# Kernel optimization log

Measured on AMD Instinct MI355X. Metric: run time of the kernel, lower is better.

The kernel has to match this reference:

```python
import jax, jax.numpy as jnp
import numpy as np

B, S, D = 4, 4096, 256

def setup_inputs() -> dict:
    key = jax.random.key(0)
    k1, k2 = jax.random.split(key)
    x = jax.random.normal(k1, (B, S, D), dtype=jnp.float32)
    # xavier_uniform for Linear(D, 2D): bound = sqrt(6/(fan_in+fan_out))
    bound = np.sqrt(6.0 / (D + 2 * D))
    W = jax.random.uniform(k2, (2 * D, D), dtype=jnp.float32, minval=-bound, maxval=bound)
    b = jnp.zeros((2 * D,), dtype=jnp.float32)
    return {"x": x, "W": W, "b": b}

def reference(x, W, b):
    # qk projection: [B,S,2D]
    qk = jnp.einsum('bsd,ed->bse', x, W) + b
    q, k = jnp.split(qk, 2, axis=-1)            # each [B,S,D]
    v = x
    scale = 1.0 / np.sqrt(D)
    logits = jnp.einsum('bqd,bkd->bqk', q, k) * scale   # [B,S,S]
    attn = jax.nn.softmax(logits, axis=-1)
    values = jnp.einsum('bqk,bkd->bqd', attn, v)        # [B,S,D]
    return values.sum(axis=1)                           # [B,D] sum-pool over queries
```

## Files before the change

kernel.cpp:

```cpp
#include <hip/hip_runtime.h>
#include <stdint.h>

typedef __bf16 v8bf __attribute__((ext_vector_type(8)));
typedef float  v4f  __attribute__((ext_vector_type(4)));
typedef int    v4i  __attribute__((ext_vector_type(4)));
typedef unsigned short u16;
typedef unsigned char  u8;

static constexpr int B_ = 4, S_ = 4096, D_ = 256, E_ = 512;
static constexpr float QSC_ = 127.0f / 4.8f;
static constexpr float DQ_  = 1.288045e-4f;

#define AS1C(p) ((const __attribute__((address_space(1))) void*)(p))
#define AS3(p)  ((__attribute__((address_space(3))) void*)(p))

__device__ __forceinline__ v8bf ldfrag(const u16* p) {
    return __builtin_bit_cast(v8bf, *(const uint4*)p);
}
__device__ __forceinline__ u16 f2bf(float f) {
    return __builtin_bit_cast(u16, (__bf16)f);
}
__device__ __forceinline__ u8 f2i8(float f) {
    float t = fminf(fmaxf(f * QSC_, -127.f), 127.f);
    return (u8)(signed char)__float2int_rn(t);
}

__global__ void k_convw(const float* __restrict__ Wf, u16* __restrict__ Wb) {
    int i = blockIdx.x * 256 + threadIdx.x;
    Wb[i] = f2bf(Wf[i]);
}

__global__ __launch_bounds__(256) void k_proj(const float* __restrict__ x,
                                              const u16* __restrict__ Wb,
                                              const float* __restrict__ bias,
                                              u8* __restrict__ Qi,
                                              u8* __restrict__ Ki) {
    const int tid = threadIdx.x, wave = tid >> 6, lane = tid & 63;
    const int l15 = lane & 15, quad = lane >> 4;
    const int tt = blockIdx.x * 2 + (wave >> 1);
    const int wsel = wave & 1;
    const int tbase = tt * 16;

    v8bf a[8];
    const float* xrow = x + (size_t)(tbase + l15) * D_ + quad * 8;
#pragma unroll
    for (int j = 0; j < 8; ++j) {
        float4 f0 = *(const float4*)(xrow + j * 32);
        float4 f1 = *(const float4*)(xrow + j * 32 + 4);
        v8bf t;
        t[0] = (__bf16)f0.x; t[1] = (__bf16)f0.y; t[2] = (__bf16)f0.z; t[3] = (__bf16)f0.w;
        t[4] = (__bf16)f1.x; t[5] = (__bf16)f1.y; t[6] = (__bf16)f1.z; t[7] = (__bf16)f1.w;
        a[j] = t;
    }

    u8* dst = wsel ? Ki : Qi;
    const u16* wbase = Wb + (size_t)(wsel * 256 + l15) * D_ + quad * 8;
    const float* bb = bias + wsel * 256;

    v8bf wcur[8], wnxt[8];
#pragma unroll
    for (int j = 0; j < 8; ++j) wcur[j] = ldfrag(wbase + j * 32);

    auto tile = [&](const v8bf (&wb)[8], int nt) {
        v4f acc = {0.f, 0.f, 0.f, 0.f};
#pragma unroll
        for (int j = 0; j < 8; ++j)
            acc = __builtin_amdgcn_mfma_f32_16x16x32_bf16(a[j], wb[j], acc, 0, 0, 0);
        const int col = nt * 16 + l15;
        const float bv = bb[col];
#pragma unroll
        for (int r = 0; r < 4; ++r) {
            const int tok = tbase + quad * 4 + r;
            dst[tok * D_ + col] = f2i8(acc[r] + bv);
        }
    };

    for (int nt = 0; nt < 16; nt += 2) {
        const u16* wp1 = wbase + (size_t)(nt + 1) * 16 * D_;
#pragma unroll
        for (int j = 0; j < 8; ++j) wnxt[j] = ldfrag(wp1 + j * 32);
        tile(wcur, nt);
        if (nt + 2 < 16) {
            const u16* wp2 = wbase + (size_t)(nt + 2) * 16 * D_;
#pragma unroll
            for (int j = 0; j < 8; ++j) wcur[j] = ldfrag(wp2 + j * 32);
        }
        tile(wnxt, nt + 1);
    }
}

__device__ __forceinline__ void stage64(const u8* src, u8* dst,
                                        int wave, int lane) {
#pragma unroll
    for (int v = 0; v < 4; ++v) {
        const int sbase = v * 256 + wave * 64;
        const int slot = sbase + lane;
        const int R = slot >> 4, P = slot & 15;
        const int c = P ^ (R & 15);
        __builtin_amdgcn_global_load_lds(AS1C(src + R * 256 + c * 16),
                                         AS3(dst + sbase * 16), 16, 0, 0);
    }
}

__global__ __launch_bounds__(256, 2) void k_passA(const u8* __restrict__ Qi,
                                                  const u8* __restrict__ Ki,
                                                  float* __restrict__ Zp) {
    __shared__ u8 sK[2][16384];
    const int tid = threadIdx.x, wave = tid >> 6, lane = tid & 63;
    const int l15 = lane & 15, quad = lane >> 4;
    const int blk = blockIdx.x;
    const int ks = blk & 7;
    const int qg = (blk >> 3) & 15;
    const int b = blk >> 7;
    const int qbase = qg * 256 + wave * 64;
    const int kstart = ks * 512;

    v4i a[4][4];
    {
        const u8* qp = Qi + (size_t)(b * S_ + qbase + l15) * D_ + quad * 16;
#pragma unroll
        for (int s = 0; s < 4; ++s)
#pragma unroll
            for (int c = 0; c < 4; ++c)
                a[s][c] = *(const v4i*)(qp + s * 16 * D_ + c * 64);
    }
    float z[4][4];
#pragma unroll
    for (int s = 0; s < 4; ++s)
#pragma unroll
        for (int r = 0; r < 4; ++r) z[s][r] = 0.f;

    const u8* kb = Ki + (size_t)(b * S_ + kstart) * D_;
    stage64(kb, sK[0], wave, lane);

    for (int t = 0; t < 8; ++t) {
        __syncthreads();
        if (t + 1 < 8) stage64(kb + (size_t)(t + 1) * 64 * D_, sK[(t + 1) & 1], wave, lane);
        const u8* base = sK[t & 1];
#pragma unroll
        for (int u = 0; u < 4; ++u) {
            v4i bf[4];
#pragma unroll
            for (int kc = 0; kc < 4; ++kc) {
                const int P = (kc * 4 + quad) ^ l15;
                bf[kc] = *(const v4i*)(base + (u * 16 + l15) * 256 + P * 16);
            }
            v4i c0 = {0,0,0,0}, c1 = {0,0,0,0}, c2 = {0,0,0,0}, c3 = {0,0,0,0};
#pragma unroll
            for (int kc = 0; kc < 4; ++kc) {
                c0 = __builtin_amdgcn_mfma_i32_16x16x64_i8(a[0][kc], bf[kc], c0, 0, 0, 0);
                c1 = __builtin_amdgcn_mfma_i32_16x16x64_i8(a[1][kc], bf[kc], c1, 0, 0, 0);
                c2 = __builtin_amdgcn_mfma_i32_16x16x64_i8(a[2][kc], bf[kc], c2, 0, 0, 0);
                c3 = __builtin_amdgcn_mfma_i32_16x16x64_i8(a[3][kc], bf[kc], c3, 0, 0, 0);
            }
#pragma unroll
            for (int r = 0; r < 4; ++r) {
                z[0][r] += __builtin_amdgcn_exp2f((float)c0[r] * DQ_);
                z[1][r] += __builtin_amdgcn_exp2f((float)c1[r] * DQ_);
                z[2][r] += __builtin_amdgcn_exp2f((float)c2[r] * DQ_);
                z[3][r] += __builtin_amdgcn_exp2f((float)c3[r] * DQ_);
            }
        }
    }

    float* zdst = Zp + (size_t)ks * B_ * S_ + b * S_ + qbase;
#pragma unroll
    for (int s = 0; s < 4; ++s)
#pragma unroll
        for (int r = 0; r < 4; ++r) {
            float v = z[s][r];
#pragma unroll
            for (int off = 1; off < 16; off <<= 1) v += __shfl_xor(v, off);
            if (l15 == 0) zdst[s * 16 + quad * 4 + r] = v;
        }
}

__global__ __launch_bounds__(256, 2) void k_passB(const u8* __restrict__ Qi,
                                                  const u8* __restrict__ Ki,
                                                  const float* __restrict__ Zp,
                                                  float* __restrict__ wp) {
    __shared__ u8 sQ[2][16384];
    __shared__ float sRZ[512];
    const int tid = threadIdx.x, wave = tid >> 6, lane = tid & 63;
    const int l15 = lane & 15, quad = lane >> 4;
    const int blk = blockIdx.x;
    const int qs = blk & 7;
    const int kg = (blk >> 3) & 15;
    const int b = blk >> 7;
    const int kbase = kg * 256 + wave * 64;
    const int qstart = qs * 512;

    v4i bk[4][4];
    {
        const u8* kp = Ki + (size_t)(b * S_ + kbase + l15) * D_ + quad * 16;
#pragma unroll
        for (int s = 0; s < 4; ++s)
#pragma unroll
            for (int c = 0; c < 4; ++c)
                bk[s][c] = *(const v4i*)(kp + s * 16 * D_ + c * 64);
    }
    float wsum[4] = {0.f, 0.f, 0.f, 0.f};

    const u8* qb = Qi + (size_t)(b * S_ + qstart) * D_;
    stage64(qb, sQ[0], wave, lane);

#pragma unroll
    for (int i = tid; i < 512; i += 256) {
        float zs = 0.f;
#pragma unroll
        for (int p = 0; p < 8; ++p)
            zs += Zp[(size_t)p * B_ * S_ + b * S_ + qstart + i];
        sRZ[i] = __builtin_amdgcn_rcpf(zs);
    }

    for (int t = 0; t < 8; ++t) {
        __syncthreads();
        if (t + 1 < 8) stage64(qb + (size_t)(t + 1) * 64 * D_, sQ[(t + 1) & 1], wave, lane);
        const u8* base = sQ[t & 1];
#pragma unroll
        for (int u = 0; u < 4; ++u) {
            const v4f rzv = *(const v4f*)(&sRZ[t * 64 + u * 16 + quad * 4]);
            v4i af[4];
#pragma unroll
            for (int kc = 0; kc < 4; ++kc) {
                const int P = (kc * 4 + quad) ^ l15;
                af[kc] = *(const v4i*)(base + (u * 16 + l15) * 256 + P * 16);
            }
            v4i c0 = {0,0,0,0}, c1 = {0,0,0,0}, c2 = {0,0,0,0}, c3 = {0,0,0,0};
#pragma unroll
            for (int kc = 0; kc < 4; ++kc) {
                c0 = __builtin_amdgcn_mfma_i32_16x16x64_i8(af[kc], bk[0][kc], c0, 0, 0, 0);
                c1 = __builtin_amdgcn_mfma_i32_16x16x64_i8(af[kc], bk[1][kc], c1, 0, 0, 0);
                c2 = __builtin_amdgcn_mfma_i32_16x16x64_i8(af[kc], bk[2][kc], c2, 0, 0, 0);
                c3 = __builtin_amdgcn_mfma_i32_16x16x64_i8(af[kc], bk[3][kc], c3, 0, 0, 0);
            }
            wsum[0] += __builtin_amdgcn_exp2f((float)c0[0] * DQ_) * rzv[0] + __builtin_amdgcn_exp2f((float)c0[1] * DQ_) * rzv[1]
                     + __builtin_amdgcn_exp2f((float)c0[2] * DQ_) * rzv[2] + __builtin_amdgcn_exp2f((float)c0[3] * DQ_) * rzv[3];
            wsum[1] += __builtin_amdgcn_exp2f((float)c1[0] * DQ_) * rzv[0] + __builtin_amdgcn_exp2f((float)c1[1] * DQ_) * rzv[1]
                     + __builtin_amdgcn_exp2f((float)c1[2] * DQ_) * rzv[2] + __builtin_amdgcn_exp2f((float)c1[3] * DQ_) * rzv[3];
            wsum[2] += __builtin_amdgcn_exp2f((float)c2[0] * DQ_) * rzv[0] + __builtin_amdgcn_exp2f((float)c2[1] * DQ_) * rzv[1]
                     + __builtin_amdgcn_exp2f((float)c2[2] * DQ_) * rzv[2] + __builtin_amdgcn_exp2f((float)c2[3] * DQ_) * rzv[3];
            wsum[3] += __builtin_amdgcn_exp2f((float)c3[0] * DQ_) * rzv[0] + __builtin_amdgcn_exp2f((float)c3[1] * DQ_) * rzv[1]
                     + __builtin_amdgcn_exp2f((float)c3[2] * DQ_) * rzv[2] + __builtin_amdgcn_exp2f((float)c3[3] * DQ_) * rzv[3];
        }
    }

    float* wdst = wp + (size_t)qs * B_ * S_ + b * S_ + kbase;
#pragma unroll
    for (int s = 0; s < 4; ++s) {
        wsum[s] += __shfl_xor(wsum[s], 16);
        wsum[s] += __shfl_xor(wsum[s], 32);
        if (quad == 0) wdst[s * 16 + l15] = wsum[s];
    }
}

__global__ __launch_bounds__(256) void k_final(const float* __restrict__ x,
                                               const float* __restrict__ wp,
                                               float* __restrict__ out) {
    const int b = blockIdx.x >> 5, kc = blockIdx.x & 31;
    const int d = threadIdx.x;
    const int k0 = kc * 128;
    float acc = 0.f;
    const float* xp = x + (size_t)(b * S_ + k0) * D_ + d;
#pragma unroll 4
    for (int kk = 0; kk < 128; ++kk) {
        float wk = 0.f;
#pragma unroll
        for (int p = 0; p < 8; ++p)
            wk += wp[(size_t)p * B_ * S_ + b * S_ + k0 + kk];
        acc += wk * xp[(size_t)kk * D_];
    }
    atomicAdd(&out[b * D_ + d], acc);
}

extern "C" void kernel_launch(void* const* d_in, const int* in_sizes, int n_in,
                              void* d_out, int out_size, void* d_ws, size_t ws_size,
                              hipStream_t stream) {
    const float* x    = (const float*)d_in[0];
    const float* W    = (const float*)d_in[1];
    const float* bias = (const float*)d_in[2];
    float* out = (float*)d_out;

    char* ws = (char*)d_ws;
    u8*    Qi = (u8*)ws;
    u8*    Ki = Qi + (size_t)B_ * S_ * D_;
    float* Zp = (float*)(ws + 8388608);
    float* wp = Zp + 8 * B_ * S_;
    u16*   Wb = (u16*)(wp + 8 * B_ * S_);

    hipMemsetAsync(out, 0, B_ * D_ * sizeof(float), stream);
    k_convw<<<E_ * D_ / 256, 256, 0, stream>>>(W, Wb);
    k_proj <<<512, 256, 0, stream>>>(x, Wb, bias, Qi, Ki);
    k_passA<<<512, 256, 0, stream>>>(Qi, Ki, Zp);
    k_passB<<<512, 256, 0, stream>>>(Qi, Ki, Zp, wp);
    k_final<<<128, 256, 0, stream>>>(x, wp, out);
}
```

Before: 165.9 us.

## Replace LDS-staged K/Q tiles with direct per-wave global register double-buffering

Both attention passes stop staging the streamed K (pass A) and Q (pass B) tiles through shared memory with global_load_lds and block barriers. Instead, each wave loads its 16-row fragments straight from global memory into registers, using a two-slot software prefetch. This removes the LDS round trip and the per-tile __syncthreads. The cost is that the four waves of a block now each fetch the same data separately, relying on L1/L2 to absorb it, and register pressure rises. Occupancy is pinned via waves_per_eu(2,2).

```diff
diff --git a/kernel.cpp b/kernel.cpp
--- a/kernel.cpp
+++ b/kernel.cpp
@@ -10,9 +10,6 @@
 static constexpr int B_ = 4, S_ = 4096, D_ = 256, E_ = 512;
 static constexpr float QSC_ = 127.0f / 4.8f;
 static constexpr float DQ_  = 1.288045e-4f;
-
-#define AS1C(p) ((const __attribute__((address_space(1))) void*)(p))
-#define AS3(p)  ((__attribute__((address_space(3))) void*)(p))
 
 __device__ __forceinline__ v8bf ldfrag(const u16* p) {
     return __builtin_bit_cast(v8bf, *(const uint4*)p);
@@ -89,23 +86,10 @@
     }
 }
 
-__device__ __forceinline__ void stage64(const u8* src, u8* dst,
-                                        int wave, int lane) {
-#pragma unroll
-    for (int v = 0; v < 4; ++v) {
-        const int sbase = v * 256 + wave * 64;
-        const int slot = sbase + lane;
-        const int R = slot >> 4, P = slot & 15;
-        const int c = P ^ (R & 15);
-        __builtin_amdgcn_global_load_lds(AS1C(src + R * 256 + c * 16),
-                                         AS3(dst + sbase * 16), 16, 0, 0);
-    }
-}
-
-__global__ __launch_bounds__(256, 2) void k_passA(const u8* __restrict__ Qi,
-                                                  const u8* __restrict__ Ki,
-                                                  float* __restrict__ Zp) {
-    __shared__ u8 sK[2][16384];
+__global__ __launch_bounds__(256)
+__attribute__((amdgpu_waves_per_eu(2, 2)))
+void k_passA(const u8* __restrict__ Qi, const u8* __restrict__ Ki,
+             float* __restrict__ Zp) {
     const int tid = threadIdx.x, wave = tid >> 6, lane = tid & 63;
     const int l15 = lane & 15, quad = lane >> 4;
     const int blk = blockIdx.x;
@@ -130,37 +114,38 @@
 #pragma unroll
         for (int r = 0; r < 4; ++r) z[s][r] = 0.f;
 
-    const u8* kb = Ki + (size_t)(b * S_ + kstart) * D_;
-    stage64(kb, sK[0], wave, lane);
-
-    for (int t = 0; t < 8; ++t) {
-        __syncthreads();
-        if (t + 1 < 8) stage64(kb + (size_t)(t + 1) * 64 * D_, sK[(t + 1) & 1], wave, lane);
-        const u8* base = sK[t & 1];
-#pragma unroll
-        for (int u = 0; u < 4; ++u) {
-            v4i bf[4];
-#pragma unroll
-            for (int kc = 0; kc < 4; ++kc) {
-                const int P = (kc * 4 + quad) ^ l15;
-                bf[kc] = *(const v4i*)(base + (u * 16 + l15) * 256 + P * 16);
-            }
-            v4i c0 = {0,0,0,0}, c1 = {0,0,0,0}, c2 = {0,0,0,0}, c3 = {0,0,0,0};
-#pragma unroll
-            for (int kc = 0; kc < 4; ++kc) {
-                c0 = __builtin_amdgcn_mfma_i32_16x16x64_i8(a[0][kc], bf[kc], c0, 0, 0, 0);
-                c1 = __builtin_amdgcn_mfma_i32_16x16x64_i8(a[1][kc], bf[kc], c1, 0, 0, 0);
-                c2 = __builtin_amdgcn_mfma_i32_16x16x64_i8(a[2][kc], bf[kc], c2, 0, 0, 0);
-                c3 = __builtin_amdgcn_mfma_i32_16x16x64_i8(a[3][kc], bf[kc], c3, 0, 0, 0);
-            }
-#pragma unroll
-            for (int r = 0; r < 4; ++r) {
-                z[0][r] += __builtin_amdgcn_exp2f((float)c0[r] * DQ_);
-                z[1][r] += __builtin_amdgcn_exp2f((float)c1[r] * DQ_);
-                z[2][r] += __builtin_amdgcn_exp2f((float)c2[r] * DQ_);
-                z[3][r] += __builtin_amdgcn_exp2f((float)c3[r] * DQ_);
-            }
-        }
+    const u8* kb = Ki + (size_t)(b * S_ + kstart + l15) * D_ + quad * 16;
+
+    v4i cur[4], nxt[4];
+    auto load = [&](v4i (&buf)[4], int t) {
+        const u8* row = kb + (size_t)t * 16 * D_;
+#pragma unroll
+        for (int c = 0; c < 4; ++c) buf[c] = *(const v4i*)(row + c * 64);
+    };
+    auto compute = [&](const v4i (&buf)[4]) {
+        v4i c0 = {0,0,0,0}, c1 = {0,0,0,0}, c2 = {0,0,0,0}, c3 = {0,0,0,0};
+#pragma unroll
+        for (int c = 0; c < 4; ++c) {
+            c0 = __builtin_amdgcn_mfma_i32_16x16x64_i8(a[0][c], buf[c], c0, 0, 0, 0);
+            c1 = __builtin_amdgcn_mfma_i32_16x16x64_i8(a[1][c], buf[c], c1, 0, 0, 0);
+            c2 = __builtin_amdgcn_mfma_i32_16x16x64_i8(a[2][c], buf[c], c2, 0, 0, 0);
+            c3 = __builtin_amdgcn_mfma_i32_16x16x64_i8(a[3][c], buf[c], c3, 0, 0, 0);
+        }
+#pragma unroll
+        for (int r = 0; r < 4; ++r) {
+            z[0][r] += __builtin_amdgcn_exp2f((float)c0[r] * DQ_);
+            z[1][r] += __builtin_amdgcn_exp2f((float)c1[r] * DQ_);
+            z[2][r] += __builtin_amdgcn_exp2f((float)c2[r] * DQ_);
+            z[3][r] += __builtin_amdgcn_exp2f((float)c3[r] * DQ_);
+        }
+    };
+
+    load(cur, 0);
+    for (int t = 0; t < 32; t += 2) {
+        load(nxt, t + 1);
+        compute(cur);
+        if (t + 2 < 32) load(cur, t + 2);
+        compute(nxt);
     }
 
     float* zdst = Zp + (size_t)ks * B_ * S_ + b * S_ + qbase;
@@ -175,11 +160,10 @@
         }
 }
 
-__global__ __launch_bounds__(256, 2) void k_passB(const u8* __restrict__ Qi,
-                                                  const u8* __restrict__ Ki,
-                                                  const float* __restrict__ Zp,
-                                                  float* __restrict__ wp) {
-    __shared__ u8 sQ[2][16384];
+__global__ __launch_bounds__(256)
+__attribute__((amdgpu_waves_per_eu(2, 2)))
+void k_passB(const u8* __restrict__ Qi, const u8* __restrict__ Ki,
+             const float* __restrict__ Zp, float* __restrict__ wp) {
     __shared__ float sRZ[512];
     const int tid = threadIdx.x, wave = tid >> 6, lane = tid & 63;
     const int l15 = lane & 15, quad = lane >> 4;
@@ -201,9 +185,6 @@
     }
     float wsum[4] = {0.f, 0.f, 0.f, 0.f};
 
-    const u8* qb = Qi + (size_t)(b * S_ + qstart) * D_;
-    stage64(qb, sQ[0], wave, lane);
-
 #pragma unroll
     for (int i = tid; i < 512; i += 256) {
         float zs = 0.f;
@@ -212,37 +193,42 @@
             zs += Zp[(size_t)p * B_ * S_ + b * S_ + qstart + i];
         sRZ[i] = __builtin_amdgcn_rcpf(zs);
     }
-
-    for (int t = 0; t < 8; ++t) {
-        __syncthreads();
-        if (t + 1 < 8) stage64(qb + (size_t)(t + 1) * 64 * D_, sQ[(t + 1) & 1], wave, lane);
-        const u8* base = sQ[t & 1];
-#pragma unroll
-        for (int u = 0; u < 4; ++u) {
-            const v4f rzv = *(const v4f*)(&sRZ[t * 64 + u * 16 + quad * 4]);
-            v4i af[4];
-#pragma unroll
-            for (int kc = 0; kc < 4; ++kc) {
-                const int P = (kc * 4 + quad) ^ l15;
-                af[kc] = *(const v4i*)(base + (u * 16 + l15) * 256 + P * 16);
-            }
-            v4i c0 = {0,0,0,0}, c1 = {0,0,0,0}, c2 = {0,0,0,0}, c3 = {0,0,0,0};
-#pragma unroll
-            for (int kc = 0; kc < 4; ++kc) {
-                c0 = __builtin_amdgcn_mfma_i32_16x16x64_i8(af[kc], bk[0][kc], c0, 0, 0, 0);
-                c1 = __builtin_amdgcn_mfma_i32_16x16x64_i8(af[kc], bk[1][kc], c1, 0, 0, 0);
-                c2 = __builtin_amdgcn_mfma_i32_16x16x64_i8(af[kc], bk[2][kc], c2, 0, 0, 0);
-                c3 = __builtin_amdgcn_mfma_i32_16x16x64_i8(af[kc], bk[3][kc], c3, 0, 0, 0);
-            }
-            wsum[0] += __builtin_amdgcn_exp2f((float)c0[0] * DQ_) * rzv[0] + __builtin_amdgcn_exp2f((float)c0[1] * DQ_) * rzv[1]
-                     + __builtin_amdgcn_exp2f((float)c0[2] * DQ_) * rzv[2] + __builtin_amdgcn_exp2f((float)c0[3] * DQ_) * rzv[3];
-            wsum[1] += __builtin_amdgcn_exp2f((float)c1[0] * DQ_) * rzv[0] + __builtin_amdgcn_exp2f((float)c1[1] * DQ_) * rzv[1]
-                     + __builtin_amdgcn_exp2f((float)c1[2] * DQ_) * rzv[2] + __builtin_amdgcn_exp2f((float)c1[3] * DQ_) * rzv[3];
-            wsum[2] += __builtin_amdgcn_exp2f((float)c2[0] * DQ_) * rzv[0] + __builtin_amdgcn_exp2f((float)c2[1] * DQ_) * rzv[1]
-                     + __builtin_amdgcn_exp2f((float)c2[2] * DQ_) * rzv[2] + __builtin_amdgcn_exp2f((float)c2[3] * DQ_) * rzv[3];
-            wsum[3] += __builtin_amdgcn_exp2f((float)c3[0] * DQ_) * rzv[0] + __builtin_amdgcn_exp2f((float)c3[1] * DQ_) * rzv[1]
-                     + __builtin_amdgcn_exp2f((float)c3[2] * DQ_) * rzv[2] + __builtin_amdgcn_exp2f((float)c3[3] * DQ_) * rzv[3];
-        }
+    __syncthreads();
+
+    const u8* qb = Qi + (size_t)(b * S_ + qstart + l15) * D_ + quad * 16;
+
+    v4i cur[4], nxt[4];
+    auto load = [&](v4i (&buf)[4], int t) {
+        const u8* row = qb + (size_t)t * 16 * D_;
+#pragma unroll
+        for (int c = 0; c < 4; ++c) buf[c] = *(const v4i*)(row + c * 64);
+    };
+    auto compute = [&](const v4i (&buf)[4], int t) {
+        v4i c0 = {0,0,0,0}, c1 = {0,0,0,0}, c2 = {0,0,0,0}, c3 = {0,0,0,0};
+#pragma unroll
+        for (int c = 0; c < 4; ++c) {
+            c0 = __builtin_amdgcn_mfma_i32_16x16x64_i8(buf[c], bk[0][c], c0, 0, 0, 0);
+            c1 = __builtin_amdgcn_mfma_i32_16x16x64_i8(buf[c], bk[1][c], c1, 0, 0, 0);
+            c2 = __builtin_amdgcn_mfma_i32_16x16x64_i8(buf[c], bk[2][c], c2, 0, 0, 0);
+            c3 = __builtin_amdgcn_mfma_i32_16x16x64_i8(buf[c], bk[3][c], c3, 0, 0, 0);
+        }
+        const v4f rzv = *(const v4f*)(&sRZ[t * 16 + quad * 4]);
+        wsum[0] += __builtin_amdgcn_exp2f((float)c0[0] * DQ_) * rzv[0] + __builtin_amdgcn_exp2f((float)c0[1] * DQ_) * rzv[1]
+                 + __builtin_amdgcn_exp2f((float)c0[2] * DQ_) * rzv[2] + __builtin_amdgcn_exp2f((float)c0[3] * DQ_) * rzv[3];
+        wsum[1] += __builtin_amdgcn_exp2f((float)c1[0] * DQ_) * rzv[0] + __builtin_amdgcn_exp2f((float)c1[1] * DQ_) * rzv[1]
+                 + __builtin_amdgcn_exp2f((float)c1[2] * DQ_) * rzv[2] + __builtin_amdgcn_exp2f((float)c1[3] * DQ_) * rzv[3];
+        wsum[2] += __builtin_amdgcn_exp2f((float)c2[0] * DQ_) * rzv[0] + __builtin_amdgcn_exp2f((float)c2[1] * DQ_) * rzv[1]
+                 + __builtin_amdgcn_exp2f((float)c2[2] * DQ_) * rzv[2] + __builtin_amdgcn_exp2f((float)c2[3] * DQ_) * rzv[3];
+        wsum[3] += __builtin_amdgcn_exp2f((float)c3[0] * DQ_) * rzv[0] + __builtin_amdgcn_exp2f((float)c3[1] * DQ_) * rzv[1]
+                 + __builtin_amdgcn_exp2f((float)c3[2] * DQ_) * rzv[2] + __builtin_amdgcn_exp2f((float)c3[3] * DQ_) * rzv[3];
+    };
+
+    load(cur, 0);
+    for (int t = 0; t < 32; t += 2) {
+        load(nxt, t + 1);
+        compute(cur, t);
+        if (t + 2 < 32) load(cur, t + 2);
+        compute(nxt, t + 1);
     }
 
     float* wdst = wp + (size_t)qs * B_ * S_ + b * S_ + kbase;
```

Result: slower. 189.1 us (+14.0%).
